# Performance work log

Hardware: AMD Instinct MI355X
Metric: run time of the kernel (lower is better)

Reference implementation:

```python
import jax, jax.numpy as jnp
import numpy as np

B, T, V, D, H = 64, 512, 32000, 512, 1024


def setup_inputs() -> dict:
    key = jax.random.key(0)
    k0, k1, k2, k3 = jax.random.split(key, 4)
    ids = jax.random.randint(k0, (B, T), 0, V)  # token id 0 is masked (mask_zero=True)
    E = jax.random.normal(k1, (V, D), jnp.float32) * 0.02
    W = jax.random.normal(k2, (D, 4 * H), jnp.float32) * (1.0 / np.sqrt(D))
    U = jax.random.normal(k3, (H, 4 * H), jnp.float32) * (1.0 / np.sqrt(H))
    b = jnp.zeros((4 * H,), jnp.float32)
    return {"input_sentances": ids, "E": E, "W": W, "U": U, "b": b}


def _encoder(ids, E, W, U, b):
    x = E[ids]                                   # [B,T,D] embedding lookup
    mask = (ids != 0)                            # [B,T] mask_zero semantics
    # Precompute input projections for all timesteps (hoisted out of the scan)
    xw = jnp.einsum('btd,dg->btg', x, W) + b     # [B,T,4H]

    def step(carry, inp):
        h, c = carry
        xw_t, m = inp                            # [B,4H], [B]
        z = xw_t + h @ U                         # [B,4H]
        i, f, g, o = jnp.split(z, 4, axis=-1)    # Keras gate order i,f,c,o
        i = jax.nn.sigmoid(i)                    # recurrent_activation
        f = jax.nn.sigmoid(f)
        g = jax.nn.sigmoid(g)                    # activation='sigmoid' (non-default!)
        o = jax.nn.sigmoid(o)
        c_new = f * c + i * g
        h_new = o * jax.nn.sigmoid(c_new)        # activation='sigmoid' on cell output too
        m = m[:, None]
        h = jnp.where(m, h_new, h)               # masked steps carry state & repeat prev output
        c = jnp.where(m, c_new, c)
        return (h, c), h

    h0 = jnp.zeros((B, H), W.dtype)
    c0 = jnp.zeros((B, H), W.dtype)
    (hF, cF), outs = jax.lax.scan(step, (h0, c0), (xw.transpose(1, 0, 2), mask.T))
    return outs.transpose(1, 0, 2), hF, cF       # (lstm_output, state_h, state_c)


def reference(input_sentances, E, W, U, b):
    return _encoder(input_sentances, E, W, U, b)
```

## Files before the change

kernel.cpp:

```cpp
#include <hip/hip_runtime.h>
#include <hip/hip_bf16.h>

typedef __bf16 bf16x8 __attribute__((ext_vector_type(8)));
typedef __bf16 bf16x4 __attribute__((ext_vector_type(4)));
typedef float  f32x4  __attribute__((ext_vector_type(4)));
typedef float  f32x16 __attribute__((ext_vector_type(16)));
typedef int    i32x4  __attribute__((ext_vector_type(4)));

#define NB 64
#define NT 512
#define ND 512
#define NH 1024
#define NG 4096

#define OFF_H   4096u
#define OFF_EB  266240u
#define OFF_WT  33034240u
#define OFF_UT  37228544u
#define OFF_XW  45617152u

#define HBUF_STRIDE 131072u

__device__ __forceinline__ void gl_lds16(const void* g, void* l) {
  typedef const unsigned __attribute__((address_space(1)))* gp_t;
  typedef unsigned __attribute__((address_space(3)))* lp_t;
  __builtin_amdgcn_global_load_lds((gp_t)g, (lp_t)l, 16, 0, 0);
}

__device__ __forceinline__ float sigf(float x) {
  return 1.0f / (1.0f + __expf(-x));
}

__device__ __forceinline__ void load_h_frags(unsigned long long a, i32x4* A) {
  asm volatile(
      "global_load_dwordx4 %0, %[a], off sc0 sc1\n\t"
      "global_load_dwordx4 %1, %[a], off offset:64 sc0 sc1\n\t"
      "global_load_dwordx4 %2, %[a], off offset:128 sc0 sc1\n\t"
      "global_load_dwordx4 %3, %[a], off offset:192 sc0 sc1\n\t"
      "global_load_dwordx4 %4, %[a], off offset:256 sc0 sc1\n\t"
      "global_load_dwordx4 %5, %[a], off offset:320 sc0 sc1\n\t"
      "global_load_dwordx4 %6, %[a], off offset:384 sc0 sc1\n\t"
      "global_load_dwordx4 %7, %[a], off offset:448 sc0 sc1\n\t"
      "s_waitcnt vmcnt(0)"
      : "=&v"(A[0]), "=&v"(A[1]), "=&v"(A[2]), "=&v"(A[3]),
        "=&v"(A[4]), "=&v"(A[5]), "=&v"(A[6]), "=&v"(A[7])
      : [a] "v"(a)
      : "memory");
}

__global__ void k_zero(uint4* p, int n) {
  int i = blockIdx.x * blockDim.x + threadIdx.x;
  int stride = gridDim.x * blockDim.x;
  uint4 z; z.x = 0; z.y = 0; z.z = 0; z.w = 0;
  for (; i < n; i += stride) p[i] = z;
}

__global__ void k_fill(uint4* p, int n) {
  int i = blockIdx.x * blockDim.x + threadIdx.x;
  int stride = gridDim.x * blockDim.x;
  uint4 s; s.x = 0xFFFFFFFFu; s.y = 0xFFFFFFFFu; s.z = 0xFFFFFFFFu; s.w = 0xFFFFFFFFu;
  for (; i < n; i += stride) p[i] = s;
}

__global__ void k_cvt(const float* __restrict__ in, __bf16* __restrict__ out, int n4) {
  int i = blockIdx.x * blockDim.x + threadIdx.x;
  int stride = gridDim.x * blockDim.x;
  for (; i < n4; i += stride) {
    float4 f = ((const float4*)in)[i];
    bf16x4 o;
    o.x = (__bf16)f.x; o.y = (__bf16)f.y; o.z = (__bf16)f.z; o.w = (__bf16)f.w;
    ((bf16x4*)out)[i] = o;
  }
}

__global__ void k_transpose(const float* __restrict__ in, __bf16* __restrict__ out,
                            int R, int C) {
  __shared__ __bf16 tile[64][72];
  int c0 = blockIdx.x * 64, r0 = blockIdx.y * 64;
  for (int i = threadIdx.x; i < 4096; i += 256) {
    int r = i >> 6, c = i & 63;
    tile[r][c] = (__bf16)in[(size_t)(r0 + r) * C + c0 + c];
  }
  __syncthreads();
  for (int i = threadIdx.x; i < 4096; i += 256) {
    int c = i >> 6, r = i & 63;
    out[(size_t)(c0 + c) * R + r0 + r] = tile[r][c];
  }
}

__global__ __launch_bounds__(256, 2) void k_gemm_xw(
    const int* __restrict__ ids, const __bf16* __restrict__ Ebf,
    const __bf16* __restrict__ Wt, const float* __restrict__ bias,
    __bf16* __restrict__ xw) {
  __shared__ __align__(16) char smem[32768];
  char* ldsA = smem;
  char* ldsB = smem + 16384;

  const int tid = threadIdx.x;
  const int lane = tid & 63, w = tid >> 6;
  const int bm = blockIdx.x >> 5;
  const int bn0 = (blockIdx.x & 31) * 128;

  const int l8r = lane >> 3, pc = lane & 7;
  size_t asrc[4], bsrc[4];
#pragma unroll
  for (int is = 0; is < 4; ++is) {
    int row = w * 32 + is * 8 + l8r;
    int id = ids[bm * 128 + row];
    asrc[is] = (size_t)id * ND + (size_t)(((pc ^ (row & 7)) * 8));
    int gn = bn0 + row;
    bsrc[is] = (size_t)gn * ND + (size_t)(((pc ^ (row & 7)) * 8));
  }

  const int rm = (w & 1) * 64, cn = (w >> 1) * 64;
  const int l31 = lane & 31, l5 = lane >> 5;
  f32x16 acc[2][2] = {};

  for (int kk = 0; kk < 8; ++kk) {
#pragma unroll
    for (int is = 0; is < 4; ++is) {
      gl_lds16(Ebf + asrc[is] + kk * 64, ldsA + w * 4096 + is * 1024);
      gl_lds16(Wt + bsrc[is] + kk * 64, ldsB + w * 4096 + is * 1024);
    }
    __syncthreads();
#pragma unroll
    for (int ksub = 0; ksub < 4; ++ksub) {
      int c = ksub * 2 + l5;
      bf16x8 af[2], bfr[2];
#pragma unroll
      for (int mt = 0; mt < 2; ++mt) {
        int row = rm + mt * 32 + l31;
        af[mt] = *(const bf16x8*)(ldsA + row * 128 + ((c ^ (row & 7)) << 4));
      }
#pragma unroll
      for (int nt = 0; nt < 2; ++nt) {
        int rowb = cn + nt * 32 + l31;
        bfr[nt] = *(const bf16x8*)(ldsB + rowb * 128 + ((c ^ (rowb & 7)) << 4));
      }
#pragma unroll
      for (int mt = 0; mt < 2; ++mt)
#pragma unroll
        for (int nt = 0; nt < 2; ++nt)
          acc[mt][nt] = __builtin_amdgcn_mfma_f32_32x32x16_bf16(
              af[mt], bfr[nt], acc[mt][nt], 0, 0, 0);
    }
    __syncthreads();
  }

#pragma unroll
  for (int nt = 0; nt < 2; ++nt) {
    int g = bn0 + cn + nt * 32 + l31;
    float bv = bias[g];
#pragma unroll
    for (int mt = 0; mt < 2; ++mt) {
#pragma unroll
      for (int r = 0; r < 16; ++r) {
        int row = (r & 3) + 8 * (r >> 2) + 4 * l5;
        int bt = bm * 128 + rm + mt * 32 + row;
        int tt = bt & 511, bb = bt >> 9;
        xw[(size_t)(tt * 64 + bb) * NG + g] = (__bf16)(acc[mt][nt][r] + bv);
      }
    }
  }
}

__global__ __launch_bounds__(256, 1) void k_lstm(
    const int* __restrict__ ids, const __bf16* __restrict__ xw,
    const __bf16* __restrict__ Ut, float* __restrict__ out,
    __bf16* __restrict__ hb) {
  extern __shared__ char dynlds[];
  float* ost = (float*)dynlds;
  float* zp  = (float*)(dynlds + 32768);

  const int tid = threadIdx.x;
  const int lane = tid & 63, w = tid >> 6;
  const int bid = blockIdx.x;
  const int ms = bid & 3, nj = bid >> 2;
  const int b0 = ms * 16, j0 = nj * 16;

  const int bn = lane & 15;
  const int kc = lane >> 4;

  bf16x8 Bf[8][4];
#pragma unroll
  for (int q = 0; q < 4; ++q) {
#pragma unroll
    for (int ks = 0; ks < 8; ++ks) {
      const __bf16* src =
          Ut + (size_t)(q * NH + j0 + bn) * NH + w * 256 + ks * 32 + kc * 8;
      gl_lds16(src, (char*)dynlds + ((w * 8 + ks) << 10));
    }
    __syncthreads();
#pragma unroll
    for (int ks = 0; ks < 8; ++ks)
      Bf[ks][q] =
          *(const bf16x8*)((char*)dynlds + (((w * 8 + ks) << 6) + lane) * 16);
    __syncthreads();
  }

  const int eb = tid >> 4, ej = tid & 15;
  const int bg = b0 + eb, jg = j0 + ej;
  float c_st = 0.0f, h_st = 0.0f;

  const int am = lane & 15;
  const unsigned long long hlane =
      (unsigned long long)(hb) + ((b0 + am) * NH + w * 256 + kc * 8) * 2ull;
  const unsigned long long hown =
      (unsigned long long)(hb) + (bg * NH + jg) * 2ull;

  unsigned offR = 0, offW = HBUF_STRIDE, offF = 2 * HBUF_STRIDE;

  const __bf16* xwp0 = xw + ((size_t)(0 * 64 + bg) << 12) + jg;
  __bf16 xr0 = xwp0[0], xr1 = xwp0[NH], xr2 = xwp0[2 * NH], xr3 = xwp0[3 * NH];
  int idv = ids[bg * NT + 0];

#pragma unroll 1
  for (int t = 0; t < NT; ++t) {
    const unsigned long long hbR = hlane + offR;

    {
      bool ok;
      do {
        i32x4 v;
        asm volatile(
            "global_load_dwordx4 %0, %[a], off sc0 sc1\n\t"
            "s_waitcnt vmcnt(0)"
            : "=&v"(v) : [a] "v"(hbR) : "memory");
        unsigned b = (unsigned)(v[0] | v[1] | v[2] | v[3]) & 0x80008000u;
        ok = __all((int)(b == 0));
      } while (!ok);
    }

    i32x4 Ar[8];
    for (;;) {
      load_h_frags(hbR, Ar);
      unsigned bad = 0;
#pragma unroll
      for (int i = 0; i < 8; ++i)
        bad |= (unsigned)(Ar[i][0] | Ar[i][1] | Ar[i][2] | Ar[i][3]);
      bad &= 0x80008000u;
      if (__all((int)(bad == 0))) break;
    }

    const int tp = (t + 1) & (NT - 1);
    const __bf16* xwn = xw + ((size_t)(tp * 64 + bg) << 12) + jg;
    __bf16 nx0 = xwn[0], nx1 = xwn[NH], nx2 = xwn[2 * NH], nx3 = xwn[3 * NH];
    int nid = ids[bg * NT + tp];

    f32x4 acc[4] = {{0, 0, 0, 0}, {0, 0, 0, 0}, {0, 0, 0, 0}, {0, 0, 0, 0}};
#pragma unroll
    for (int ks = 0; ks < 8; ++ks) {
      bf16x8 a = __builtin_bit_cast(bf16x8, Ar[ks]);
#pragma unroll
      for (int q = 0; q < 4; ++q)
        acc[q] = __builtin_amdgcn_mfma_f32_16x16x32_bf16(a, Bf[ks][q], acc[q], 0, 0, 0);
    }

#pragma unroll
    for (int q = 0; q < 4; ++q)
#pragma unroll
      for (int r = 0; r < 4; ++r)
        zp[(w * 4 + q) * 272 + (kc * 4 + r) * 17 + bn] = acc[q][r];
    __syncthreads();

    {
      unsigned sv = 0xFFFFu;
      unsigned long long fa = hown + offF;
      asm volatile(
          "global_store_short %[a], %[d], off sc0 sc1"
          :: [a] "v"(fa), [d] "v"(sv) : "memory");
    }

    float z0 = 0, z1 = 0, z2 = 0, z3 = 0;
#pragma unroll
    for (int wv = 0; wv < 4; ++wv) {
      z0 += zp[(wv * 4 + 0) * 272 + eb * 17 + ej];
      z1 += zp[(wv * 4 + 1) * 272 + eb * 17 + ej];
      z2 += zp[(wv * 4 + 2) * 272 + eb * 17 + ej];
      z3 += zp[(wv * 4 + 3) * 272 + eb * 17 + ej];
    }
    z0 += (float)xr0; z1 += (float)xr1; z2 += (float)xr2; z3 += (float)xr3;
    float iv = sigf(z0), fv = sigf(z1), gv = sigf(z2), ov = sigf(z3);
    float cn = fv * c_st + iv * gv;
    float hn = ov * sigf(cn);
    bool m = (idv != 0);
    c_st = m ? cn : c_st;
    h_st = m ? hn : h_st;

    ost[(t & 31) * 256 + tid] = h_st;

    asm volatile("s_waitcnt vmcnt(0)" ::: "memory");

    {
      unsigned hv = (unsigned)__builtin_bit_cast(unsigned short, (__bf16)h_st);
      unsigned long long ha = hown + offW;
      asm volatile(
          "global_store_short %[a], %[d], off sc0 sc1"
          :: [a] "v"(ha), [d] "v"(hv) : "memory");
    }

    if ((t & 31) == 31) {
      float* ob = out + (size_t)bg * (NT * NH) + (size_t)(t - 31) * NH + jg;
#pragma unroll
      for (int s = 0; s < 32; ++s)
        ob[(size_t)s * NH] = ost[s * 256 + tid];
    }

    __syncthreads();

    unsigned tmp = offR; offR = offW; offW = offF; offF = tmp;
    xr0 = nx0; xr1 = nx1; xr2 = nx2; xr3 = nx3; idv = nid;
  }

  out[33554432u + bg * NH + jg] = h_st;
  out[33554432u + 65536u + bg * NH + jg] = c_st;
}

extern "C" void kernel_launch(void* const* d_in, const int* in_sizes, int n_in,
                              void* d_out, int out_size, void* d_ws, size_t ws_size,
                              hipStream_t stream) {
  const int* ids = (const int*)d_in[0];
  const float* E = (const float*)d_in[1];
  const float* W = (const float*)d_in[2];
  const float* U = (const float*)d_in[3];
  const float* bias = (const float*)d_in[4];
  char* ws = (char*)d_ws;
  __bf16* Ebf = (__bf16*)(ws + OFF_EB);
  __bf16* Wt = (__bf16*)(ws + OFF_WT);
  __bf16* Ut = (__bf16*)(ws + OFF_UT);
  __bf16* xw = (__bf16*)(ws + OFF_XW);
  __bf16* hb = (__bf16*)(ws + OFF_H);
  float* out = (float*)d_out;

  (void)hipFuncSetAttribute((const void*)k_lstm,
                            hipFuncAttributeMaxDynamicSharedMemorySize, 50176);

  hipLaunchKernelGGL(k_zero, dim3(32), dim3(256), 0, stream, (uint4*)(ws + OFF_H), 8192);
  hipLaunchKernelGGL(k_fill, dim3(32), dim3(256), 0, stream,
                     (uint4*)(ws + OFF_H + HBUF_STRIDE), 8192);
  hipLaunchKernelGGL(k_cvt, dim3(2048), dim3(256), 0, stream, E, Ebf, 4096000);
  hipLaunchKernelGGL(k_transpose, dim3(64, 8), dim3(256), 0, stream, W, Wt, 512, 4096);
  hipLaunchKernelGGL(k_transpose, dim3(64, 16), dim3(256), 0, stream, U, Ut, 1024, 4096);
  hipLaunchKernelGGL(k_gemm_xw, dim3(8192), dim3(256), 0, stream, ids, Ebf, Wt, bias, xw);
  hipLaunchKernelGGL(k_fill, dim3(32), dim3(256), 0, stream,
                     (uint4*)(ws + OFF_H + 2 * HBUF_STRIDE), 8192);
  hipLaunchKernelGGL(k_lstm, dim3(256), dim3(256), 50176, stream, ids, xw, Ut, out, hb);
}
```

Measured before the change: 1.773 ms.

## Replace poison-flag h-buffer handshake with parity-tagged h values in LSTM recurrence

```diff
diff --git a/kernel.cpp b/kernel.cpp
--- a/kernel.cpp
+++ b/kernel.cpp
@@ -210,6 +210,9 @@
 
   unsigned offR = 0, offW = HBUF_STRIDE, offF = 2 * HBUF_STRIDE;
 
+  const int parE = ((eb >> 2) ^ eb) & 1;
+  const int rbase = eb * 32 + (parE << 4) + ej;
+
   const __bf16* xwp0 = xw + ((size_t)(0 * 64 + bg) << 12) + jg;
   __bf16 xr0 = xwp0[0], xr1 = xwp0[NH], xr2 = xwp0[2 * NH], xr3 = xwp0[3 * NH];
   int idv = ids[bg * NT + 0];
@@ -217,8 +220,17 @@
 #pragma unroll 1
   for (int t = 0; t < NT; ++t) {
     const unsigned long long hbR = hlane + offR;
-
-    {
+    const unsigned expectTag = (t & 1) ? 0x80008000u : 0u;
+
+    i32x4 Ar[8];
+    for (;;) {
+      load_h_frags(hbR, Ar);
+      unsigned bad = 0;
+#pragma unroll
+      for (int i = 0; i < 8; ++i)
+        bad |= (unsigned)((Ar[i][0] ^ (int)expectTag) | (Ar[i][1] ^ (int)expectTag) |
+                          (Ar[i][2] ^ (int)expectTag) | (Ar[i][3] ^ (int)expectTag));
+      if (__all((int)((bad & 0x80008000u) == 0))) break;
       bool ok;
       do {
         i32x4 v;
@@ -226,26 +238,27 @@
             "global_load_dwordx4 %0, %[a], off sc0 sc1\n\t"
             "s_waitcnt vmcnt(0)"
             : "=&v"(v) : [a] "v"(hbR) : "memory");
-        unsigned b = (unsigned)(v[0] | v[1] | v[2] | v[3]) & 0x80008000u;
-        ok = __all((int)(b == 0));
+        unsigned b = (unsigned)((v[0] ^ (int)expectTag) | (v[1] ^ (int)expectTag) |
+                                (v[2] ^ (int)expectTag) | (v[3] ^ (int)expectTag));
+        ok = __all((int)((b & 0x80008000u) == 0));
       } while (!ok);
-    }
-
-    i32x4 Ar[8];
-    for (;;) {
-      load_h_frags(hbR, Ar);
-      unsigned bad = 0;
-#pragma unroll
-      for (int i = 0; i < 8; ++i)
-        bad |= (unsigned)(Ar[i][0] | Ar[i][1] | Ar[i][2] | Ar[i][3]);
-      bad &= 0x80008000u;
-      if (__all((int)(bad == 0))) break;
     }
 
     const int tp = (t + 1) & (NT - 1);
     const __bf16* xwn = xw + ((size_t)(tp * 64 + bg) << 12) + jg;
-    __bf16 nx0 = xwn[0], nx1 = xwn[NH], nx2 = xwn[2 * NH], nx3 = xwn[3 * NH];
+    __bf16 nx0 = __builtin_nontemporal_load(xwn);
+    __bf16 nx1 = __builtin_nontemporal_load(xwn + NH);
+    __bf16 nx2 = __builtin_nontemporal_load(xwn + 2 * NH);
+    __bf16 nx3 = __builtin_nontemporal_load(xwn + 3 * NH);
     int nid = ids[bg * NT + tp];
+
+    if (t & 1) {
+#pragma unroll
+      for (int i = 0; i < 8; ++i) {
+        Ar[i][0] &= 0x7FFF7FFF; Ar[i][1] &= 0x7FFF7FFF;
+        Ar[i][2] &= 0x7FFF7FFF; Ar[i][3] &= 0x7FFF7FFF;
+      }
+    }
 
     f32x4 acc[4] = {{0, 0, 0, 0}, {0, 0, 0, 0}, {0, 0, 0, 0}, {0, 0, 0, 0}};
 #pragma unroll
@@ -260,24 +273,17 @@
     for (int q = 0; q < 4; ++q)
 #pragma unroll
       for (int r = 0; r < 4; ++r)
-        zp[(w * 4 + q) * 272 + (kc * 4 + r) * 17 + bn] = acc[q][r];
-    __syncthreads();
-
-    {
-      unsigned sv = 0xFFFFu;
-      unsigned long long fa = hown + offF;
-      asm volatile(
-          "global_store_short %[a], %[d], off sc0 sc1"
-          :: [a] "v"(fa), [d] "v"(sv) : "memory");
-    }
+        zp[((w * 4 + q) << 9) + ((kc * 4 + r) << 5) + (((kc ^ r) & 1) << 4) + bn] =
+            acc[q][r];
+    __syncthreads();
 
     float z0 = 0, z1 = 0, z2 = 0, z3 = 0;
 #pragma unroll
     for (int wv = 0; wv < 4; ++wv) {
-      z0 += zp[(wv * 4 + 0) * 272 + eb * 17 + ej];
-      z1 += zp[(wv * 4 + 1) * 272 + eb * 17 + ej];
-      z2 += zp[(wv * 4 + 2) * 272 + eb * 17 + ej];
-      z3 += zp[(wv * 4 + 3) * 272 + eb * 17 + ej];
+      z0 += zp[((wv * 4 + 0) << 9) + rbase];
+      z1 += zp[((wv * 4 + 1) << 9) + rbase];
+      z2 += zp[((wv * 4 + 2) << 9) + rbase];
+      z3 += zp[((wv * 4 + 3) << 9) + rbase];
     }
     z0 += (float)xr0; z1 += (float)xr1; z2 += (float)xr2; z3 += (float)xr3;
     float iv = sigf(z0), fv = sigf(z1), gv = sigf(z2), ov = sigf(z3);
@@ -287,23 +293,21 @@
     c_st = m ? cn : c_st;
     h_st = m ? hn : h_st;
 
-    ost[(t & 31) * 256 + tid] = h_st;
-
-    asm volatile("s_waitcnt vmcnt(0)" ::: "memory");
-
     {
-      unsigned hv = (unsigned)__builtin_bit_cast(unsigned short, (__bf16)h_st);
+      unsigned hv = (unsigned)__builtin_bit_cast(unsigned short, (__bf16)h_st) |
+                    ((unsigned)((t + 1) & 1) << 15);
       unsigned long long ha = hown + offW;
       asm volatile(
           "global_store_short %[a], %[d], off sc0 sc1"
           :: [a] "v"(ha), [d] "v"(hv) : "memory");
     }
 
+    ost[(t & 31) * 256 + tid] = h_st;
     if ((t & 31) == 31) {
       float* ob = out + (size_t)bg * (NT * NH) + (size_t)(t - 31) * NH + jg;
 #pragma unroll
       for (int s = 0; s < 32; ++s)
-        ob[(size_t)s * NH] = ost[s * 256 + tid];
+        __builtin_nontemporal_store(ost[s * 256 + tid], ob + (size_t)s * NH);
     }
 
     __syncthreads();
@@ -333,16 +337,14 @@
   float* out = (float*)d_out;
 
   (void)hipFuncSetAttribute((const void*)k_lstm,
-                            hipFuncAttributeMaxDynamicSharedMemorySize, 50176);
-
-  hipLaunchKernelGGL(k_zero, dim3(32), dim3(256), 0, stream, (uint4*)(ws + OFF_H), 8192);
-  hipLaunchKernelGGL(k_fill, dim3(32), dim3(256), 0, stream,
-                     (uint4*)(ws + OFF_H + HBUF_STRIDE), 8192);
+                            hipFuncAttributeMaxDynamicSharedMemorySize, 65536);
+
+  hipLaunchKernelGGL(k_zero, dim3(64), dim3(256), 0, stream, (uint4*)(ws + OFF_H), 16384);
   hipLaunchKernelGGL(k_cvt, dim3(2048), dim3(256), 0, stream, E, Ebf, 4096000);
   hipLaunchKernelGGL(k_transpose, dim3(64, 8), dim3(256), 0, stream, W, Wt, 512, 4096);
   hipLaunchKernelGGL(k_transpose, dim3(64, 16), dim3(256), 0, stream, U, Ut, 1024, 4096);
   hipLaunchKernelGGL(k_gemm_xw, dim3(8192), dim3(256), 0, stream, ids, Ebf, Wt, bias, xw);
   hipLaunchKernelGGL(k_fill, dim3(32), dim3(256), 0, stream,
                      (uint4*)(ws + OFF_H + 2 * HBUF_STRIDE), 8192);
-  hipLaunchKernelGGL(k_lstm, dim3(256), dim3(256), 50176, stream, ids, xw, Ut, out, hb);
-}
+  hipLaunchKernelGGL(k_lstm, dim3(256), dim3(256), 65536, stream, ids, xw, Ut, out, hb);
+}
```

Result: slower. 2.339 ms (+31.9%).
